# Kernel optimization log

Measured on AMD Instinct MI355X. Metric: run time of the kernel, lower is better.

The kernel has to match this reference:

```python
import jax, jax.numpy as jnp
import numpy as np

N_ELEC = 62      # electrodes per graph (fixed by RGNN/SEED)
BATCH = 4096     # number of graphs
IN_CH = 5
HID = 32
N_CLS = 3
K = 2            # SGConv propagation steps (num_layers)


def setup_inputs() -> dict:
    key = jax.random.key(0)
    k1, k2, k3, k4 = jax.random.split(key, 4)
    n_tril = N_ELEC * (N_ELEC + 1) // 2  # 1953 learned lower-tri weights
    x = jax.random.normal(k1, (BATCH * N_ELEC, IN_CH), jnp.float32)
    adj_tril = jax.random.uniform(k2, (n_tril,), jnp.float32)
    lin_w = jax.random.normal(k3, (HID, IN_CH), jnp.float32) * 0.3
    lin_b = jnp.zeros((HID,), jnp.float32)
    fc_w = jax.random.normal(k4, (N_CLS, HID), jnp.float32) * 0.2
    fc_b = jnp.zeros((N_CLS,), jnp.float32)
    # Dense per-graph edge list matching adj.reshape(-1).repeat(B):
    # edge e = b*3844 + i*62 + j has source row=b*62+i, target col=b*62+j.
    i = np.arange(N_ELEC, dtype=np.int32)
    src = np.repeat(i, N_ELEC)              # [3844]
    dst = np.tile(i, N_ELEC)                # [3844]
    off = (np.arange(BATCH, dtype=np.int32) * N_ELEC)[:, None]
    row = (src[None, :] + off).reshape(-1)  # [B*3844]
    col = (dst[None, :] + off).reshape(-1)
    edge_index = jnp.asarray(np.stack([row, col]))  # int32 [2, E]
    batch_idx = jnp.asarray(np.repeat(np.arange(BATCH, dtype=np.int32), N_ELEC))
    return dict(x=x, adj_tril=adj_tril, lin_w=lin_w, lin_b=lin_b,
                fc_w=fc_w, fc_b=fc_b, edge_index=edge_index, batch_idx=batch_idx)


def reference(x, adj_tril, lin_w, lin_b, fc_w, fc_b, edge_index, batch_idx):
    # Rebuild symmetric dense adjacency from learned lower-triangular params.
    xs, ys = np.tril_indices(N_ELEC)  # static indices
    A = jnp.zeros((N_ELEC, N_ELEC), x.dtype).at[xs, ys].set(adj_tril)
    A = A + A.T - jnp.diag(jnp.diag(A))
    w = jnp.tile(A.reshape(-1), BATCH)        # edge weights [E]
    row, col = edge_index[0], edge_index[1]
    n_nodes = BATCH * N_ELEC
    # Symmetric GCN norm: D^-1/2 A D^-1/2 over the edge list (self-loops
    # already present in the dense graph, so add_remaining_self_loops is a
    # pure edge reorder here).
    deg = jax.ops.segment_sum(jnp.abs(w), row, num_segments=n_nodes)
    safe_deg = jnp.where(deg > 0, deg, 1.0)
    dinv = jnp.where(deg > 0, jax.lax.rsqrt(safe_deg), 0.0)
    norm = dinv[row] * w * dinv[col]          # [E]
    # K rounds of gather-scale-scatter propagation (SGConv).
    h = x
    for _ in range(K):
        h = jax.ops.segment_sum(norm[:, None] * h[row], col, num_segments=n_nodes)
    h = jax.nn.relu(h @ lin_w.T + lin_b)       # SGConv linear + relu
    pooled = jax.ops.segment_sum(h, batch_idx, num_segments=BATCH)  # global_add_pool
    # dropout is identity in eval mode
    return pooled @ fc_w.T + fc_b              # [B, num_classes]
```

## Files before the change

kernel.cpp:

```cpp
#include <hip/hip_runtime.h>


#define NE 62
#define IC 5
#define NTRIL 1953
#define SA 68
#define MTOT 3844

__global__ __launch_bounds__(256) void build_M(const float* __restrict__ adj_tril,
                                               float* __restrict__ Mg) {
    __shared__ float A[NE * SA];
    __shared__ float dinv[NE];
    int tid = threadIdx.x;
    for (int t = tid; t < NTRIL; t += 256) {
        float v = adj_tril[t];
        float r = sqrtf((float)(8 * t + 1));
        int i = (int)((r - 1.0f) * 0.5f);
        while ((i + 1) * (i + 2) / 2 <= t) ++i;
        while (i * (i + 1) / 2 > t) --i;
        int j = t - i * (i + 1) / 2;
        A[i * SA + j] = v;
        A[j * SA + i] = v;
    }
    __syncthreads();
    if (tid < NE) {
        float s = 0.f;
        for (int k = 0; k < NE; ++k) s += fabsf(A[tid * SA + k]);
        dinv[tid] = (s > 0.f) ? rsqrtf(s) : 0.f;
    }
    __syncthreads();
    for (int g = tid; g < NE * NE; g += 256) {
        int i = g / NE, j = g % NE;
        A[i * SA + j] *= dinv[i] * dinv[j];
    }
    __syncthreads();
    int g = blockIdx.x * 256 + tid;
    if (g < NE * NE) {
        int r = g / NE, cidx = g % NE;
        const float4* ra = (const float4*)(A + r * SA);
        const float4* rb = (const float4*)(A + cidx * SA);
        float acc = 0.f;
#pragma unroll
        for (int c = 0; c < 15; ++c) {
            float4 a = ra[c], b = rb[c];
            acc += a.x * b.x + a.y * b.y + a.z * b.z + a.w * b.w;
        }
        acc += A[r * SA + 60] * A[cidx * SA + 60] + A[r * SA + 61] * A[cidx * SA + 61];
        int addr = (cidx < 60) ? ((cidx >> 2) * 248 + r * 4 + (cidx & 3))
                               : (3720 + r * 2 + (cidx - 60));
        Mg[addr] = acc;
    }
}

__global__ __launch_bounds__(256) void forward_k(const float* __restrict__ x,
        const float* __restrict__ lin_w, const float* __restrict__ lin_b,
        const float* __restrict__ fc_w, const float* __restrict__ fc_b,
        const float* __restrict__ Mg, float* __restrict__ out) {
    __shared__ float Xs[4 * 312];
    __shared__ float Ys[4][NE * 12];
    int tid = threadIdx.x;
    {
        const float2* xsrc = (const float2*)(x + (size_t)blockIdx.x * (4 * 310));
        for (int t = tid; t < 620; t += 256) {
            int w = t / 155, o = t - w * 155;
            *(float2*)&Xs[w * 312 + o * 2] = xsrc[t];
        }
    }
    int wid = tid >> 6;
    int lane = tid & 63;
    int b = blockIdx.x * 4 + wid;
    int c = lane & 31;
    float w0 = lin_w[c * 5 + 0], w1 = lin_w[c * 5 + 1], w2 = lin_w[c * 5 + 2],
          w3 = lin_w[c * 5 + 3], w4 = lin_w[c * 5 + 4];
    float lb = lin_b[c];
    float f0 = fc_w[c], f1 = fc_w[32 + c], f2 = fc_w[64 + c];
    __syncthreads();
    int j = lane;
    if (j < NE) {
        const float* xb = Xs + wid * 312;
        float y0 = 0, y1 = 0, y2 = 0, y3 = 0, y4 = 0;
#pragma unroll
        for (int ch = 0; ch < 15; ++ch) {
            float4 m = *(const float4*)(Mg + ch * 248 + j * 4);
            const float4* xi = (const float4*)(xb + ch * 20);
            float4 xa = xi[0], xv = xi[1], xc = xi[2], xd = xi[3], xe = xi[4];
            y0 += m.x * xa.x; y1 += m.x * xa.y; y2 += m.x * xa.z; y3 += m.x * xa.w; y4 += m.x * xv.x;
            y0 += m.y * xv.y; y1 += m.y * xv.z; y2 += m.y * xv.w; y3 += m.y * xc.x; y4 += m.y * xc.y;
            y0 += m.z * xc.z; y1 += m.z * xc.w; y2 += m.z * xd.x; y3 += m.z * xd.y; y4 += m.z * xd.z;
            y0 += m.w * xd.w; y1 += m.w * xe.x; y2 += m.w * xe.y; y3 += m.w * xe.z; y4 += m.w * xe.w;
        }
        float2 mt = *(const float2*)(Mg + 3720 + j * 2);
        const float* xt = xb + 300;
        y0 += mt.x * xt[0] + mt.y * xt[5];
        y1 += mt.x * xt[1] + mt.y * xt[6];
        y2 += mt.x * xt[2] + mt.y * xt[7];
        y3 += mt.x * xt[3] + mt.y * xt[8];
        y4 += mt.x * xt[4] + mt.y * xt[9];
        float* yr = &Ys[wid][j * 12];
        *(float4*)yr = make_float4(y0, y1, y2, y3);
        yr[4] = y4;
    }
    __syncthreads();
    int half = lane >> 5;
    float acc = 0.f;
    int jbeg = half * 31;
    for (int t = 0; t < 31; ++t) {
        const float* yr = &Ys[wid][(jbeg + t) * 12];
        float4 yv = *(const float4*)yr;
        float d = yv.x * w0 + yv.y * w1 + yv.z * w2 + yv.w * w3 + yr[4] * w4 + lb;
        acc += fmaxf(d, 0.f);
    }
    acc += __shfl_xor(acc, 32, 64);
    float p0 = acc * f0, p1 = acc * f1, p2 = acc * f2;
#pragma unroll
    for (int m = 16; m >= 1; m >>= 1) {
        p0 += __shfl_xor(p0, m, 64);
        p1 += __shfl_xor(p1, m, 64);
        p2 += __shfl_xor(p2, m, 64);
    }
    if (lane == 0) {
        out[b * 3 + 0] = p0 + fc_b[0];
        out[b * 3 + 1] = p1 + fc_b[1];
        out[b * 3 + 2] = p2 + fc_b[2];
    }
}

extern "C" void kernel_launch(void* const* d_in, const int* in_sizes, int n_in,
                              void* d_out, int out_size, void* d_ws, size_t ws_size,
                              hipStream_t stream) {
    const float* x        = (const float*)d_in[0];
    const float* adj_tril = (const float*)d_in[1];
    const float* lin_w    = (const float*)d_in[2];
    const float* lin_b    = (const float*)d_in[3];
    const float* fc_w     = (const float*)d_in[4];
    const float* fc_b     = (const float*)d_in[5];
    float* out = (float*)d_out;
    float* Mg  = (float*)d_ws;

    build_M<<<16, 256, 0, stream>>>(adj_tril, Mg);
    forward_k<<<1024, 256, 0, stream>>>(x, lin_w, lin_b, fc_w, fc_b, Mg, out);
}
```

Measured before the change: 181.8 us.

## Fuse adjacency build into forward kernel, propagate twice instead of squaring

Drops the separate build_M kernel and its workspace round-trip. Each block now rebuilds the symmetric adjacency and degree normalisation in shared memory, folds the D^-1/2 scaling into the features, and applies A twice (with a dinv^2 scale between passes) instead of precomputing M = Â². This saves a kernel launch and the global read of M, but every block repeats the 1953-element adjacency build and degree reduction, and runs two propagation passes with extra barriers and more shared memory.

```diff
diff --git a/kernel.cpp b/kernel.cpp
--- a/kernel.cpp
+++ b/kernel.cpp
@@ -2,16 +2,30 @@
 
 
 #define NE 62
-#define IC 5
 #define NTRIL 1953
-#define SA 68
-#define MTOT 3844
+#define SA 66
 
-__global__ __launch_bounds__(256) void build_M(const float* __restrict__ adj_tril,
-                                               float* __restrict__ Mg) {
-    __shared__ float A[NE * SA];
-    __shared__ float dinv[NE];
+__global__ __launch_bounds__(256) void fused_k(const float* __restrict__ x,
+        const float* __restrict__ adj_tril,
+        const float* __restrict__ lin_w, const float* __restrict__ lin_b,
+        const float* __restrict__ fc_w, const float* __restrict__ fc_b,
+        float* __restrict__ out) {
+    __shared__ __align__(16) float A2[NE * SA];
+    __shared__ float dinv[NE], dinv2[NE];
+    __shared__ float Rp[NE * 4];
+    __shared__ __align__(16) float Xs[4 * 312];
+    __shared__ __align__(16) float Y1[4 * 312];
+    __shared__ __align__(16) float Ys[4][NE * 12];
     int tid = threadIdx.x;
+    int bid = blockIdx.x;
+
+    {
+        const float2* xsrc = (const float2*)(x + (size_t)bid * (4 * 310));
+        for (int t = tid; t < 620; t += 256) {
+            int w = t / 155, o = t - w * 155;
+            *(float2*)&Xs[w * 312 + o * 2] = xsrc[t];
+        }
+    }
     for (int t = tid; t < NTRIL; t += 256) {
         float v = adj_tril[t];
         float r = sqrtf((float)(8 * t + 1));
@@ -19,86 +33,104 @@
         while ((i + 1) * (i + 2) / 2 <= t) ++i;
         while (i * (i + 1) / 2 > t) --i;
         int j = t - i * (i + 1) / 2;
-        A[i * SA + j] = v;
-        A[j * SA + i] = v;
+        A2[i * SA + j] = v;
+        A2[j * SA + i] = v;
+    }
+    __syncthreads();
+    if (tid < NE * 4) {
+        int row = tid >> 2, q = tid & 3;
+        int c0 = q * 16, cnt = (q == 3) ? 14 : 16;
+        const float* ar = A2 + row * SA + c0;
+        float s = 0.f;
+        for (int k = 0; k < cnt; ++k) s += fabsf(ar[k]);
+        Rp[tid] = s;
     }
     __syncthreads();
     if (tid < NE) {
-        float s = 0.f;
-        for (int k = 0; k < NE; ++k) s += fabsf(A[tid * SA + k]);
-        dinv[tid] = (s > 0.f) ? rsqrtf(s) : 0.f;
+        float deg = Rp[tid * 4] + Rp[tid * 4 + 1] + Rp[tid * 4 + 2] + Rp[tid * 4 + 3];
+        float di = (deg > 0.f) ? rsqrtf(deg) : 0.f;
+        dinv[tid] = di;
+        dinv2[tid] = di * di;
     }
     __syncthreads();
-    for (int g = tid; g < NE * NE; g += 256) {
-        int i = g / NE, j = g % NE;
-        A[i * SA + j] *= dinv[i] * dinv[j];
-    }
-    __syncthreads();
-    int g = blockIdx.x * 256 + tid;
-    if (g < NE * NE) {
-        int r = g / NE, cidx = g % NE;
-        const float4* ra = (const float4*)(A + r * SA);
-        const float4* rb = (const float4*)(A + cidx * SA);
-        float acc = 0.f;
-#pragma unroll
-        for (int c = 0; c < 15; ++c) {
-            float4 a = ra[c], b = rb[c];
-            acc += a.x * b.x + a.y * b.y + a.z * b.z + a.w * b.w;
-        }
-        acc += A[r * SA + 60] * A[cidx * SA + 60] + A[r * SA + 61] * A[cidx * SA + 61];
-        int addr = (cidx < 60) ? ((cidx >> 2) * 248 + r * 4 + (cidx & 3))
-                               : (3720 + r * 2 + (cidx - 60));
-        Mg[addr] = acc;
-    }
-}
-
-__global__ __launch_bounds__(256) void forward_k(const float* __restrict__ x,
-        const float* __restrict__ lin_w, const float* __restrict__ lin_b,
-        const float* __restrict__ fc_w, const float* __restrict__ fc_b,
-        const float* __restrict__ Mg, float* __restrict__ out) {
-    __shared__ float Xs[4 * 312];
-    __shared__ float Ys[4][NE * 12];
-    int tid = threadIdx.x;
-    {
-        const float2* xsrc = (const float2*)(x + (size_t)blockIdx.x * (4 * 310));
-        for (int t = tid; t < 620; t += 256) {
-            int w = t / 155, o = t - w * 155;
-            *(float2*)&Xs[w * 312 + o * 2] = xsrc[t];
-        }
+    for (int t = tid; t < 1240; t += 256) {
+        int w = t / 310, o = t - w * 310;
+        int i = o / 5;
+        Xs[w * 312 + o] *= dinv[i];
     }
     int wid = tid >> 6;
     int lane = tid & 63;
-    int b = blockIdx.x * 4 + wid;
+    int b = bid * 4 + wid;
     int c = lane & 31;
     float w0 = lin_w[c * 5 + 0], w1 = lin_w[c * 5 + 1], w2 = lin_w[c * 5 + 2],
           w3 = lin_w[c * 5 + 3], w4 = lin_w[c * 5 + 4];
     float lb = lin_b[c];
     float f0 = fc_w[c], f1 = fc_w[32 + c], f2 = fc_w[64 + c];
     __syncthreads();
+
     int j = lane;
+    const float* arow = A2 + j * SA;
     if (j < NE) {
         const float* xb = Xs + wid * 312;
         float y0 = 0, y1 = 0, y2 = 0, y3 = 0, y4 = 0;
 #pragma unroll
         for (int ch = 0; ch < 15; ++ch) {
-            float4 m = *(const float4*)(Mg + ch * 248 + j * 4);
+            float2 a01 = *(const float2*)(arow + 4 * ch);
+            float2 a23 = *(const float2*)(arow + 4 * ch + 2);
             const float4* xi = (const float4*)(xb + ch * 20);
             float4 xa = xi[0], xv = xi[1], xc = xi[2], xd = xi[3], xe = xi[4];
-            y0 += m.x * xa.x; y1 += m.x * xa.y; y2 += m.x * xa.z; y3 += m.x * xa.w; y4 += m.x * xv.x;
-            y0 += m.y * xv.y; y1 += m.y * xv.z; y2 += m.y * xv.w; y3 += m.y * xc.x; y4 += m.y * xc.y;
-            y0 += m.z * xc.z; y1 += m.z * xc.w; y2 += m.z * xd.x; y3 += m.z * xd.y; y4 += m.z * xd.z;
-            y0 += m.w * xd.w; y1 += m.w * xe.x; y2 += m.w * xe.y; y3 += m.w * xe.z; y4 += m.w * xe.w;
+            y0 += a01.x * xa.x; y1 += a01.x * xa.y; y2 += a01.x * xa.z; y3 += a01.x * xa.w; y4 += a01.x * xv.x;
+            y0 += a01.y * xv.y; y1 += a01.y * xv.z; y2 += a01.y * xv.w; y3 += a01.y * xc.x; y4 += a01.y * xc.y;
+            y0 += a23.x * xc.z; y1 += a23.x * xc.w; y2 += a23.x * xd.x; y3 += a23.x * xd.y; y4 += a23.x * xd.z;
+            y0 += a23.y * xd.w; y1 += a23.y * xe.x; y2 += a23.y * xe.y; y3 += a23.y * xe.z; y4 += a23.y * xe.w;
         }
-        float2 mt = *(const float2*)(Mg + 3720 + j * 2);
-        const float* xt = xb + 300;
-        y0 += mt.x * xt[0] + mt.y * xt[5];
-        y1 += mt.x * xt[1] + mt.y * xt[6];
-        y2 += mt.x * xt[2] + mt.y * xt[7];
-        y3 += mt.x * xt[3] + mt.y * xt[8];
-        y4 += mt.x * xt[4] + mt.y * xt[9];
+        {
+            float2 a = *(const float2*)(arow + 60);
+            const float* xt = xb + 300;
+            float2 t0 = *(const float2*)(xt + 0), t1 = *(const float2*)(xt + 2);
+            float2 t2 = *(const float2*)(xt + 4), t3 = *(const float2*)(xt + 6);
+            float2 t4 = *(const float2*)(xt + 8);
+            y0 += a.x * t0.x + a.y * t2.y;
+            y1 += a.x * t0.y + a.y * t3.x;
+            y2 += a.x * t1.x + a.y * t3.y;
+            y3 += a.x * t1.y + a.y * t4.x;
+            y4 += a.x * t2.x + a.y * t4.y;
+        }
+        float s = dinv2[j];
+        float* yw = &Y1[wid * 312 + j * 5];
+        yw[0] = y0 * s; yw[1] = y1 * s; yw[2] = y2 * s; yw[3] = y3 * s; yw[4] = y4 * s;
+    }
+    __syncthreads();
+    if (j < NE) {
+        const float* xb = Y1 + wid * 312;
+        float y0 = 0, y1 = 0, y2 = 0, y3 = 0, y4 = 0;
+#pragma unroll
+        for (int ch = 0; ch < 15; ++ch) {
+            float2 a01 = *(const float2*)(arow + 4 * ch);
+            float2 a23 = *(const float2*)(arow + 4 * ch + 2);
+            const float4* xi = (const float4*)(xb + ch * 20);
+            float4 xa = xi[0], xv = xi[1], xc = xi[2], xd = xi[3], xe = xi[4];
+            y0 += a01.x * xa.x; y1 += a01.x * xa.y; y2 += a01.x * xa.z; y3 += a01.x * xa.w; y4 += a01.x * xv.x;
+            y0 += a01.y * xv.y; y1 += a01.y * xv.z; y2 += a01.y * xv.w; y3 += a01.y * xc.x; y4 += a01.y * xc.y;
+            y0 += a23.x * xc.z; y1 += a23.x * xc.w; y2 += a23.x * xd.x; y3 += a23.x * xd.y; y4 += a23.x * xd.z;
+            y0 += a23.y * xd.w; y1 += a23.y * xe.x; y2 += a23.y * xe.y; y3 += a23.y * xe.z; y4 += a23.y * xe.w;
+        }
+        {
+            float2 a = *(const float2*)(arow + 60);
+            const float* xt = xb + 300;
+            float2 t0 = *(const float2*)(xt + 0), t1 = *(const float2*)(xt + 2);
+            float2 t2 = *(const float2*)(xt + 4), t3 = *(const float2*)(xt + 6);
+            float2 t4 = *(const float2*)(xt + 8);
+            y0 += a.x * t0.x + a.y * t2.y;
+            y1 += a.x * t0.y + a.y * t3.x;
+            y2 += a.x * t1.x + a.y * t3.y;
+            y3 += a.x * t1.y + a.y * t4.x;
+            y4 += a.x * t2.x + a.y * t4.y;
+        }
+        float s = dinv[j];
         float* yr = &Ys[wid][j * 12];
-        *(float4*)yr = make_float4(y0, y1, y2, y3);
-        yr[4] = y4;
+        *(float4*)yr = make_float4(y0 * s, y1 * s, y2 * s, y3 * s);
+        yr[4] = y4 * s;
     }
     __syncthreads();
     int half = lane >> 5;
@@ -135,8 +167,6 @@
     const float* fc_w     = (const float*)d_in[4];
     const float* fc_b     = (const float*)d_in[5];
     float* out = (float*)d_out;
-    float* Mg  = (float*)d_ws;
 
-    build_M<<<16, 256, 0, stream>>>(adj_tril, Mg);
-    forward_k<<<1024, 256, 0, stream>>>(x, lin_w, lin_b, fc_w, fc_b, Mg, out);
+    fused_k<<<1024, 256, 0, stream>>>(x, adj_tril, lin_w, lin_b, fc_w, fc_b, out);
 }
```

Result: no change. 184.8 us (+1.7%).
